# Optimization experiments

Hardware: AMD Instinct MI355X
Metric: run time of the kernel (lower is better)

Reference implementation:

```python
import jax, jax.numpy as jnp
import numpy as np

HIDDEN = 512
NHEADS = 8
ALPHA = 0.1
NUM_HOP = 4
MASK_VAL = -16384.0
LN_EPS = 1e-5


def setup_inputs() -> dict:
    key = jax.random.key(0)
    ks = jax.random.split(key, 10)
    B, N, H = 8, 1024, HIDDEN
    s = 1.0 / np.sqrt(H)
    x = jax.random.normal(ks[0], (B, N, H), dtype=jnp.float32)
    adj = jax.random.randint(ks[1], (B, N, N), 0, 2, dtype=jnp.int32)
    Wq = jax.random.uniform(ks[2], (H, H), jnp.float32, -s, s)
    bq = jax.random.uniform(ks[3], (H,), jnp.float32, -s, s)
    Wk = jax.random.uniform(ks[4], (H, H), jnp.float32, -s, s)
    bk = jax.random.uniform(ks[5], (H,), jnp.float32, -s, s)
    Wv = jax.random.uniform(ks[6], (H, H), jnp.float32, -s, s)
    bv = jax.random.uniform(ks[7], (H,), jnp.float32, -s, s)
    gamma = jnp.ones((H,), jnp.float32)
    beta = jnp.zeros((H,), jnp.float32)
    return {"x": x, "adj": adj, "Wq": Wq, "bq": bq, "Wk": Wk, "bk": bk,
            "Wv": Wv, "bv": bv, "gamma": gamma, "beta": beta}


def reference(x, adj, Wq, bq, Wk, bk, Wv, bv, gamma, beta):
    B, N, H = x.shape
    u = H // NHEADS
    # torch Linear: y = x @ W^T + b
    q = x @ Wq.T + bq  # [B,N,H]
    k = x @ Wk.T + bk
    v = x @ Wv.T + bv
    # split hidden into contiguous head chunks (matches per-head slicing)
    qh = q.reshape(B, N, NHEADS, u).transpose(0, 2, 1, 3)  # [B,Hd,N,u]
    kh = k.reshape(B, N, NHEADS, u).transpose(0, 2, 1, 3)
    vh = v.reshape(B, N, NHEADS, u).transpose(0, 2, 1, 3)
    scores = jnp.einsum('bhnd,bhmd->bhnm', qh, kh)  # [B,Hd,N,N]
    mask = (adj == 0)[:, None, :, :]  # broadcast over heads
    scores = jnp.where(mask, MASK_VAL, scores)
    pros = jax.nn.softmax(scores, axis=-1)
    z_init = vh
    z = z_init
    for _ in range(NUM_HOP):
        z = (1.0 - ALPHA) * jnp.einsum('bhnm,bhmd->bhnd', pros, z) + ALPHA * z_init
    h_prime = z.transpose(0, 2, 1, 3).reshape(B, N, H)  # concat heads
    y = x + h_prime
    mu = jnp.mean(y, axis=-1, keepdims=True)
    var = jnp.mean((y - mu) ** 2, axis=-1, keepdims=True)
    return (y - mu) / jnp.sqrt(var + LN_EPS) * gamma + beta
```

## Files before the change

### kernel.cpp

```cpp
#include <hip/hip_runtime.h>
#include <hip/hip_bf16.h>

#define BB 8
#define NN 1024
#define HH 512
#define NHEADS 8
#define UU 64

typedef __attribute__((ext_vector_type(8))) short short8;
typedef __attribute__((ext_vector_type(4))) float f32x4;
typedef __attribute__((ext_vector_type(16))) float f32x16;
typedef unsigned short u16;
typedef unsigned char u8;

__device__ inline float b2f(unsigned short u) {
    union { float f; unsigned int i; } c; c.i = ((unsigned int)u) << 16; return c.f;
}
__device__ inline unsigned short f2b(float f) {
    __hip_bfloat16 h = __float2bfloat16(f);
    return *reinterpret_cast<unsigned short*>(&h);
}
__device__ inline void gl_lds16(const void* g, void* l) {
    __builtin_amdgcn_global_load_lds(
        (const __attribute__((address_space(1))) unsigned int*)g,
        (__attribute__((address_space(3))) unsigned int*)l, 16, 0, 0);
}

__global__ __launch_bounds__(256) void cvt_w(
    const float* __restrict__ Wq, const float* __restrict__ Wk,
    const float* __restrict__ Wv, u16* __restrict__ Wb)
{
    const int which = blockIdx.y;
    const float* src = which == 0 ? Wq : (which == 1 ? Wk : Wv);
    u16* dst = Wb + (size_t)which * HH * HH;
    const int base = (blockIdx.x * 256 + threadIdx.x) * 8;
    const float4* sp = (const float4*)&src[base];
    float4 a = sp[0], b = sp[1];
    short8 o;
    o[0] = (short)f2b(a.x); o[1] = (short)f2b(a.y);
    o[2] = (short)f2b(a.z); o[3] = (short)f2b(a.w);
    o[4] = (short)f2b(b.x); o[5] = (short)f2b(b.y);
    o[6] = (short)f2b(b.z); o[7] = (short)f2b(b.w);
    *(short8*)&dst[base] = o;
}

__global__ __launch_bounds__(256) void adj_pack(
    const int* __restrict__ adj, unsigned int* __restrict__ adjpT)
{
    const int wave = threadIdx.x >> 6, lane = threadIdx.x & 63;
    const int row = blockIdx.x * 4 + wave;
    const int b = row >> 10, r = row & 1023;
    const int* ar = adj + (size_t)row * NN;
    unsigned int* ob = adjpT + (((size_t)b) << 15) + r;
    #pragma unroll
    for (int it = 0; it < 16; ++it) {
        int a = ar[it * 64 + lane];
        unsigned long long m = __ballot(a != 0);
        if (lane == 0) {
            ob[(size_t)(2 * it)     << 10] = (unsigned int)m;
            ob[(size_t)(2 * it + 1) << 10] = (unsigned int)(m >> 32);
        }
    }
}

__global__ __launch_bounds__(256) void qkv_gemm(
    const float* __restrict__ x, const u16* __restrict__ Wb,
    const float* __restrict__ bq, const float* __restrict__ bk,
    const float* __restrict__ bv,
    u16* __restrict__ q, u16* __restrict__ k, u16* __restrict__ v)
{
    const int which = blockIdx.z;
    const u16* W      = Wb + (size_t)which * HH * HH;
    const float* bias = which == 0 ? bq : (which == 1 ? bk : bv);
    u16* out          = which == 0 ? q  : (which == 1 ? k  : v);

    const int tid = threadIdx.x;
    const int wave = tid >> 6, lane = tid & 63;
    const int ln = lane & 15, quad = lane >> 4;
    const int wr = (wave >> 1) * 64, wc = (wave & 1) * 64;
    const int rowbase = blockIdx.x * 128, colbase = blockIdx.y * 128;

    __shared__ __align__(16) u16 As[128 * 40];
    __shared__ __align__(16) u16 Bs[128 * 32];
    __shared__ __align__(16) u16 Cs[128 * 136];

    f32x4 acc[4][4];
    #pragma unroll
    for (int ri = 0; ri < 4; ++ri)
        #pragma unroll
        for (int ci = 0; ci < 4; ++ci) acc[ri][ci] = (f32x4){0.f, 0.f, 0.f, 0.f};

    const int lr = lane >> 2;
    const int sg = lane & 3;

    for (int kk = 0; kk < HH; kk += 32) {
        __syncthreads();
        #pragma unroll
        for (int i = 0; i < 2; ++i) {
            int r = wave * 32 + i * 16 + lr;
            const float* xp = &x[(size_t)(rowbase + r) * HH + kk + sg * 8];
            float4 f0 = *(const float4*)xp, f1 = *(const float4*)(xp + 4);
            short8 o;
            o[0] = (short)f2b(f0.x); o[1] = (short)f2b(f0.y);
            o[2] = (short)f2b(f0.z); o[3] = (short)f2b(f0.w);
            o[4] = (short)f2b(f1.x); o[5] = (short)f2b(f1.y);
            o[6] = (short)f2b(f1.z); o[7] = (short)f2b(f1.w);
            *(short8*)&As[r * 40 + sg * 8] = o;
            gl_lds16(&W[(size_t)(colbase + r) * HH + kk + sg * 8],
                     (char*)Bs + (wave * 32 + i * 16) * 64);
        }
        __syncthreads();

        short8 bfr[4];
        #pragma unroll
        for (int ci = 0; ci < 4; ++ci)
            bfr[ci] = *(const short8*)&Bs[(wc + ci * 16 + ln) * 32 + quad * 8];
        #pragma unroll
        for (int ri = 0; ri < 4; ++ri) {
            short8 af = *(const short8*)&As[(wr + ri * 16 + ln) * 40 + quad * 8];
            #pragma unroll
            for (int ci = 0; ci < 4; ++ci)
                acc[ri][ci] = __builtin_amdgcn_mfma_f32_16x16x32_bf16(af, bfr[ci], acc[ri][ci], 0, 0, 0);
        }
    }

    #pragma unroll
    for (int ci = 0; ci < 4; ++ci) {
        int col = wc + ci * 16 + ln;
        float bb = bias[colbase + col];
        #pragma unroll
        for (int ri = 0; ri < 4; ++ri) {
            #pragma unroll
            for (int r = 0; r < 4; ++r) {
                int row = wr + ri * 16 + quad * 4 + r;
                Cs[row * 136 + col] = f2b(acc[ri][ci][r] + bb);
            }
        }
    }
    __syncthreads();
    {
        int row = tid >> 1, half = tid & 1;
        int gcol0 = colbase + half * 64;
        int hh = gcol0 >> 6;
        int grow = rowbase + row;
        int bidx = grow >> 10, n = grow & 1023;
        u16* op = &out[(((size_t)(bidx * NHEADS + hh)) * NN + n) * UU];
        const u16* cp = &Cs[row * 136 + half * 64];
        #pragma unroll
        for (int j = 0; j < 8; ++j)
            *(short8*)(op + j * 8) = *(const short8*)(cp + j * 8);
    }
}

__global__ __launch_bounds__(256) void vt8(
    const u16* __restrict__ v, u8* __restrict__ v8t)
{
    const int bh = blockIdx.x >> 2, part = blockIdx.x & 3;
    const int t = threadIdx.x;
    const size_t hd = (size_t)bh << 16;
    __shared__ u16 tile[64][72];

    for (int chunk = part * 4; chunk < part * 4 + 4; ++chunk) {
        const int n0 = chunk * 64;
        const int r = t >> 2, cs = t & 3;
        const u16* vp = &v[((size_t)bh * NN + n0 + r) * UU + cs * 16];
        short8 a = *(const short8*)vp;
        short8 b8 = *(const short8*)(vp + 8);
        #pragma unroll
        for (int j = 0; j < 8; ++j) {
            tile[r][cs * 16 + j] = (u16)a[j];
            tile[r][cs * 16 + 8 + j] = (u16)b8[j];
        }
        __syncthreads();
        const int c = t & 63, qt = t >> 6;
        unsigned int w[4];
        #pragma unroll
        for (int g = 0; g < 4; ++g) {
            float f0 = b2f(tile[qt * 16 + g * 4 + 0][c]);
            float f1 = b2f(tile[qt * 16 + g * 4 + 1][c]);
            float f2 = b2f(tile[qt * 16 + g * 4 + 2][c]);
            float f3 = b2f(tile[qt * 16 + g * 4 + 3][c]);
            int lo = __builtin_amdgcn_cvt_pk_fp8_f32(f0, f1, 0, false);
            w[g] = (unsigned int)__builtin_amdgcn_cvt_pk_fp8_f32(f2, f3, lo, true);
        }
        uint4 o; o.x = w[0]; o.y = w[1]; o.z = w[2]; o.w = w[3];
        *(uint4*)&v8t[hd + (size_t)c * 1024 + n0 + qt * 16] = o;
        __syncthreads();
    }
}

__device__ inline f32x16 score_tile(const u16* kp, unsigned int m2,
                                    const short8* qf)
{
    short8 kf[4];
    #pragma unroll
    for (int f = 0; f < 4; ++f) kf[f] = *(const short8*)(kp + f * 16);
    f32x16 acc;
    #pragma unroll
    for (int j = 0; j < 16; ++j) {
        const int koff = (j & 3) + 8 * (j >> 2);
        acc[j] = ((m2 >> koff) & 1u) ? -32.0f : -16384.0f;
    }
    #pragma unroll
    for (int f = 0; f < 4; ++f)
        acc = __builtin_amdgcn_mfma_f32_32x32x16_bf16(kf[f], qf[f], acc, 0, 0, 0);
    return acc;
}

__global__ __launch_bounds__(256) void scores_softmax(
    const u16* __restrict__ q, const u16* __restrict__ kmat,
    const unsigned int* __restrict__ adjpT, u8* __restrict__ P8)
{
    const int b = blockIdx.z, h = blockIdx.y;
    const int bh = b * NHEADS + h;
    const int tid = threadIdx.x;
    const int wave = tid >> 6, lane = tid & 63;
    const int l31 = lane & 31, hi = lane >> 5;
    const int rg = wave >> 1, kh = wave & 1;
    const int n = (blockIdx.x * 2 + rg) * 32 + l31;
    const int kt0 = kh * 16, kt1 = kt0 + 16;

    __shared__ float rs[2][2][32];

    short8 qf[4];
    const u16* qp = &q[((size_t)bh * NN + n) * UU + hi * 8];
    #pragma unroll
    for (int f = 0; f < 4; ++f) qf[f] = *(const short8*)(qp + f * 16);

    const u16* kbase = kmat + (size_t)bh * NN * UU + hi * 8;
    const unsigned int* mbase = adjpT + (((size_t)b) << 15) + n;

    float rsum = 0.f;
    #pragma unroll 2
    for (int t = kt0; t < kt1; ++t) {
        const unsigned int m2 = mbase[(size_t)t << 10] >> (4 * hi);
        const u16* kp = kbase + (size_t)(t * 32 + l31) * UU;
        f32x16 acc = score_tile(kp, m2, qf);
        #pragma unroll
        for (int j = 0; j < 16; ++j) rsum += __expf(acc[j]);
    }
    rsum += __shfl_xor(rsum, 32);
    if (lane < 32) rs[rg][kh][lane] = rsum;
    __syncthreads();
    const float scl = 16.0f / (rs[rg][0][l31] + rs[rg][1][l31]);

    u8* pb = P8 + (((size_t)bh) << 20) + (size_t)(n >> 4) * 16384
           + (n & 15) * 32 + hi * 4;
    #pragma unroll 2
    for (int t = kt0; t < kt1; ++t) {
        const unsigned int m2 = mbase[(size_t)t << 10] >> (4 * hi);
        const u16* kp = kbase + (size_t)(t * 32 + l31) * UU;
        f32x16 acc = score_tile(kp, m2, qf);
        u8* pt = pb + (size_t)t * 512;
        #pragma unroll
        for (int g = 0; g < 4; ++g) {
            float e0 = __expf(acc[g * 4 + 0]) * scl;
            float e1 = __expf(acc[g * 4 + 1]) * scl;
            float e2 = __expf(acc[g * 4 + 2]) * scl;
            float e3 = __expf(acc[g * 4 + 3]) * scl;
            int lo = __builtin_amdgcn_cvt_pk_fp8_f32(e0, e1, 0, false);
            unsigned int dw = (unsigned int)__builtin_amdgcn_cvt_pk_fp8_f32(e2, e3, lo, true);
            *(unsigned int*)(pt + g * 8) = dw;
        }
    }
}

__global__ __launch_bounds__(512) void hop(
    const u8* __restrict__ P8, const u8* __restrict__ z8in,
    const u16* __restrict__ v, u8* __restrict__ z8out,
    u16* __restrict__ zbf_out, int last)
{
    const int b = blockIdx.z, h = blockIdx.y, rt = blockIdx.x;
    const int bh = b * NHEADS + h;
    const int tid = threadIdx.x;
    const int wave = tid >> 6, lane = tid & 63;
    const int ln = lane & 15, quad = lane >> 4;
    const int wrow = rt * 128 + wave * 16;

    __shared__ __align__(16) u8 zt[64 * 1040];

    const u8* zg = z8in + ((size_t)bh << 16);
    #pragma unroll
    for (int i = 0; i < 8; ++i) {
        int c = wave * 8 + i;
        gl_lds16(zg + (size_t)c * 1024 + lane * 16, (char*)zt + c * 1040);
    }
    __syncthreads();

    f32x4 acc[4];
    #pragma unroll
    for (int ci = 0; ci < 4; ++ci) acc[ci] = (f32x4){0.f, 0.f, 0.f, 0.f};

    const u8* pt = P8 + ((size_t)bh << 20) + (size_t)(rt * 8 + wave) * 16384
                 + ln * 32 + quad * 8;
    #pragma unroll 4
    for (int kc = 0; kc < 32; ++kc) {
        long a = *(const long*)(pt + kc * 512);
        int kk = kc * 32;
        #pragma unroll
        for (int ci = 0; ci < 4; ++ci) {
            long bz = *(const long*)&zt[(ci * 16 + ln) * 1040 + kk + quad * 8];
            acc[ci] = __builtin_amdgcn_mfma_f32_16x16x32_fp8_fp8(a, bz, acc[ci], 0, 0, 0);
        }
    }

    if (last) {
        #pragma unroll
        for (int ci = 0; ci < 4; ++ci) {
            int col = ci * 16 + ln;
            #pragma unroll
            for (int r = 0; r < 4; ++r) {
                int row = wrow + quad * 4 + r;
                float vv = b2f(v[((size_t)bh * NN + row) * UU + col]);
                zbf_out[((size_t)(b * NN + row)) * HH + h * UU + col]
                    = f2b(0.05625f * acc[ci][r] + 0.1f * vv);
            }
        }
    } else {
        u8* zo = z8out + ((size_t)bh << 16);
        #pragma unroll
        for (int ci = 0; ci < 4; ++ci) {
            int col = ci * 16 + ln;
            float zv[4];
            #pragma unroll
            for (int r = 0; r < 4; ++r) {
                int row = wrow + quad * 4 + r;
                float vv = b2f(v[((size_t)bh * NN + row) * UU + col]);
                zv[r] = 0.05625f * acc[ci][r] + 0.1f * vv;
            }
            int lo = __builtin_amdgcn_cvt_pk_fp8_f32(zv[0], zv[1], 0, false);
            unsigned int dw = (unsigned int)__builtin_amdgcn_cvt_pk_fp8_f32(zv[2], zv[3], lo, true);
            *(unsigned int*)&zo[(size_t)col * 1024 + wrow + quad * 4] = dw;
        }
    }
}

__global__ __launch_bounds__(256) void resid_ln(
    const float* __restrict__ x, const u16* __restrict__ z,
    const float* __restrict__ gamma, const float* __restrict__ beta,
    float* __restrict__ out)
{
    const int r = blockIdx.x * 4 + (threadIdx.x >> 6);
    const int lane = threadIdx.x & 63;
    const size_t base = (size_t)r * HH + lane * 8;

    const float4* xp = (const float4*)&x[base];
    float4 x0 = xp[0], x1 = xp[1];
    short8 zv = *(const short8*)&z[base];
    float y[8];
    y[0] = x0.x + b2f((u16)zv[0]); y[1] = x0.y + b2f((u16)zv[1]);
    y[2] = x0.z + b2f((u16)zv[2]); y[3] = x0.w + b2f((u16)zv[3]);
    y[4] = x1.x + b2f((u16)zv[4]); y[5] = x1.y + b2f((u16)zv[5]);
    y[6] = x1.z + b2f((u16)zv[6]); y[7] = x1.w + b2f((u16)zv[7]);

    float s = 0.f, sq = 0.f;
    #pragma unroll
    for (int j = 0; j < 8; ++j) { s += y[j]; sq += y[j] * y[j]; }
    #pragma unroll
    for (int off = 32; off >= 1; off >>= 1) {
        s  += __shfl_xor(s, off);
        sq += __shfl_xor(sq, off);
    }
    const float mu = s * (1.0f / HH);
    const float var = sq * (1.0f / HH) - mu * mu;
    const float rstd = rsqrtf(var + 1e-5f);

    const float4* gp = (const float4*)&gamma[lane * 8];
    const float4* bp = (const float4*)&beta[lane * 8];
    float4 g0 = gp[0], g1 = gp[1], b0 = bp[0], b1 = bp[1];

    float4 o0, o1;
    o0.x = (y[0] - mu) * rstd * g0.x + b0.x;
    o0.y = (y[1] - mu) * rstd * g0.y + b0.y;
    o0.z = (y[2] - mu) * rstd * g0.z + b0.z;
    o0.w = (y[3] - mu) * rstd * g0.w + b0.w;
    o1.x = (y[4] - mu) * rstd * g1.x + b1.x;
    o1.y = (y[5] - mu) * rstd * g1.y + b1.y;
    o1.z = (y[6] - mu) * rstd * g1.z + b1.z;
    o1.w = (y[7] - mu) * rstd * g1.w + b1.w;
    float4* op = (float4*)&out[base];
    op[0] = o0; op[1] = o1;
}

extern "C" void kernel_launch(void* const* d_in, const int* in_sizes, int n_in,
                              void* d_out, int out_size, void* d_ws, size_t ws_size,
                              hipStream_t stream)
{
    const float* x   = (const float*)d_in[0];
    const int* adj   = (const int*)d_in[1];
    const float* Wq  = (const float*)d_in[2];
    const float* bq  = (const float*)d_in[3];
    const float* Wk  = (const float*)d_in[4];
    const float* bk  = (const float*)d_in[5];
    const float* Wv  = (const float*)d_in[6];
    const float* bv  = (const float*)d_in[7];
    const float* gamma = (const float*)d_in[8];
    const float* beta  = (const float*)d_in[9];
    float* out = (float*)d_out;

    const size_t E = (size_t)BB * NN * HH;
    u16* ws16 = (u16*)d_ws;
    u16* q  = ws16 + E;
    u16* k  = ws16 + 2 * E;
    u16* v  = ws16 + 3 * E;
    u16* za = ws16 + 4 * E;
    u16* Wb = ws16 + 5 * E;
    u8* base8 = (u8*)(ws16 + 5 * E + 786432);
    u8* P8  = base8;
    u8* z8a = base8 + ((size_t)64 << 20);
    u8* z8b = z8a + ((size_t)4 << 20);
    u8* v8t = z8b + ((size_t)4 << 20);
    unsigned int* adjpT = (unsigned int*)(v8t + ((size_t)4 << 20));

    cvt_w<<<dim3(128, 3), 256, 0, stream>>>(Wq, Wk, Wv, Wb);
    adj_pack<<<dim3(2048), 256, 0, stream>>>(adj, adjpT);
    qkv_gemm<<<dim3(64, 4, 3), 256, 0, stream>>>(x, Wb, bq, bk, bv, q, k, v);
    vt8<<<dim3(256), 256, 0, stream>>>(v, v8t);
    scores_softmax<<<dim3(16, NHEADS, BB), 256, 0, stream>>>(q, k, adjpT, P8);
    hop<<<dim3(8, NHEADS, BB), 512, 0, stream>>>(P8, v8t, v, z8a, za, 0);
    hop<<<dim3(8, NHEADS, BB), 512, 0, stream>>>(P8, z8a, v, z8b, za, 0);
    hop<<<dim3(8, NHEADS, BB), 512, 0, stream>>>(P8, z8b, v, z8a, za, 0);
    hop<<<dim3(8, NHEADS, BB), 512, 0, stream>>>(P8, z8a, v, z8b, za, 1);
    resid_ln<<<dim3(2048), 256, 0, stream>>>(x, za, gamma, beta, out);
}
```

Baseline: 301.0 us.

## Split softmax rows across four key-quarter waves and use exp2 with folded scaling

The scores_softmax kernel now assigns one 32-row tile per block and splits the keys across four waves instead of two. Each wave preloads its mask words once into registers. The mask and scaling are folded into a single fma+exp2, with the normalisation applied in log space (offset minus log of the row sum), which removes the per-element multiply. Partial sums go into four independent accumulators, and the grid doubles to 32 blocks per head, with a launch bound asking for 8 blocks per CU. This raises parallelism and cuts ALU work, at the cost of more blocks and a log-domain normalisation that slightly changes the rounding.

```diff
diff --git a/kernel.cpp b/kernel.cpp
--- a/kernel.cpp
+++ b/kernel.cpp
@@ -189,77 +189,93 @@
     }
 }
 
-__device__ inline f32x16 score_tile(const u16* kp, unsigned int m2,
-                                    const short8* qf)
+__device__ inline f32x16 score_tile(const u16* kp, const short8* qf)
 {
     short8 kf[4];
     #pragma unroll
     for (int f = 0; f < 4; ++f) kf[f] = *(const short8*)(kp + f * 16);
     f32x16 acc;
     #pragma unroll
-    for (int j = 0; j < 16; ++j) {
-        const int koff = (j & 3) + 8 * (j >> 2);
-        acc[j] = ((m2 >> koff) & 1u) ? -32.0f : -16384.0f;
-    }
+    for (int j = 0; j < 16; ++j) acc[j] = 0.f;
     #pragma unroll
     for (int f = 0; f < 4; ++f)
         acc = __builtin_amdgcn_mfma_f32_32x32x16_bf16(kf[f], qf[f], acc, 0, 0, 0);
     return acc;
 }
 
-__global__ __launch_bounds__(256) void scores_softmax(
+__global__ __launch_bounds__(256, 8) void scores_softmax(
     const u16* __restrict__ q, const u16* __restrict__ kmat,
     const unsigned int* __restrict__ adjpT, u8* __restrict__ P8)
 {
     const int b = blockIdx.z, h = blockIdx.y;
     const int bh = b * NHEADS + h;
     const int tid = threadIdx.x;
-    const int wave = tid >> 6, lane = tid & 63;
+    const int kq = tid >> 6, lane = tid & 63;
     const int l31 = lane & 31, hi = lane >> 5;
-    const int rg = wave >> 1, kh = wave & 1;
-    const int n = (blockIdx.x * 2 + rg) * 32 + l31;
-    const int kt0 = kh * 16, kt1 = kt0 + 16;
-
-    __shared__ float rs[2][2][32];
+    const int n = blockIdx.x * 32 + l31;
+    const int kt0 = kq * 8;
+
+    __shared__ float rs[4][32];
 
     short8 qf[4];
     const u16* qp = &q[((size_t)bh * NN + n) * UU + hi * 8];
     #pragma unroll
     for (int f = 0; f < 4; ++f) qf[f] = *(const short8*)(qp + f * 16);
 
-    const u16* kbase = kmat + (size_t)bh * NN * UU + hi * 8;
+    const u16* kbase = kmat + (size_t)bh * NN * UU + (size_t)(kt0 * 32 + l31) * UU + hi * 8;
     const unsigned int* mbase = adjpT + (((size_t)b) << 15) + n;
 
-    float rsum = 0.f;
+    unsigned int mv[8];
+    #pragma unroll
+    for (int i = 0; i < 8; ++i)
+        mv[i] = mbase[(size_t)(kt0 + i) << 10] >> (4 * hi);
+
+    const float L2E = 1.442695041f;
+    const float C0 = -46.16624f;
+    const float CM = -100000.0f;
+
+    float rs0 = 0.f, rs1 = 0.f, rs2 = 0.f, rs3 = 0.f;
     #pragma unroll 2
-    for (int t = kt0; t < kt1; ++t) {
-        const unsigned int m2 = mbase[(size_t)t << 10] >> (4 * hi);
-        const u16* kp = kbase + (size_t)(t * 32 + l31) * UU;
-        f32x16 acc = score_tile(kp, m2, qf);
-        #pragma unroll
-        for (int j = 0; j < 16; ++j) rsum += __expf(acc[j]);
-    }
+    for (int i = 0; i < 8; ++i) {
+        f32x16 acc = score_tile(kbase + (size_t)i * (32 * UU), qf);
+        const unsigned int m2 = mv[i];
+        #pragma unroll
+        for (int g = 0; g < 4; ++g) {
+            #pragma unroll
+            for (int r = 0; r < 4; ++r) {
+                const int koff = r + 8 * g;
+                float addv = ((m2 >> koff) & 1u) ? C0 : CM;
+                float e = __builtin_amdgcn_exp2f(fmaf(L2E, acc[g * 4 + r], addv));
+                if (g == 0) rs0 += e; else if (g == 1) rs1 += e;
+                else if (g == 2) rs2 += e; else rs3 += e;
+            }
+        }
+    }
+    float rsum = (rs0 + rs1) + (rs2 + rs3);
     rsum += __shfl_xor(rsum, 32);
-    if (lane < 32) rs[rg][kh][lane] = rsum;
+    if (lane < 32) rs[kq][lane] = rsum;
     __syncthreads();
-    const float scl = 16.0f / (rs[rg][0][l31] + rs[rg][1][l31]);
+    const float total = (rs[0][l31] + rs[1][l31]) + (rs[2][l31] + rs[3][l31]);
+    const float lscl = -42.16624f - __builtin_amdgcn_logf(total);
 
     u8* pb = P8 + (((size_t)bh) << 20) + (size_t)(n >> 4) * 16384
            + (n & 15) * 32 + hi * 4;
     #pragma unroll 2
-    for (int t = kt0; t < kt1; ++t) {
-        const unsigned int m2 = mbase[(size_t)t << 10] >> (4 * hi);
-        const u16* kp = kbase + (size_t)(t * 32 + l31) * UU;
-        f32x16 acc = score_tile(kp, m2, qf);
-        u8* pt = pb + (size_t)t * 512;
+    for (int i = 0; i < 8; ++i) {
+        f32x16 acc = score_tile(kbase + (size_t)i * (32 * UU), qf);
+        const unsigned int m2 = mv[i];
+        u8* pt = pb + (size_t)(kt0 + i) * 512;
         #pragma unroll
         for (int g = 0; g < 4; ++g) {
-            float e0 = __expf(acc[g * 4 + 0]) * scl;
-            float e1 = __expf(acc[g * 4 + 1]) * scl;
-            float e2 = __expf(acc[g * 4 + 2]) * scl;
-            float e3 = __expf(acc[g * 4 + 3]) * scl;
-            int lo = __builtin_amdgcn_cvt_pk_fp8_f32(e0, e1, 0, false);
-            unsigned int dw = (unsigned int)__builtin_amdgcn_cvt_pk_fp8_f32(e2, e3, lo, true);
+            float e[4];
+            #pragma unroll
+            for (int r = 0; r < 4; ++r) {
+                const int koff = r + 8 * g;
+                float addv = ((m2 >> koff) & 1u) ? lscl : CM;
+                e[r] = __builtin_amdgcn_exp2f(fmaf(L2E, acc[g * 4 + r], addv));
+            }
+            int lo = __builtin_amdgcn_cvt_pk_fp8_f32(e[0], e[1], 0, false);
+            unsigned int dw = (unsigned int)__builtin_amdgcn_cvt_pk_fp8_f32(e[2], e[3], lo, true);
             *(unsigned int*)(pt + g * 8) = dw;
         }
     }
@@ -416,7 +432,7 @@
     adj_pack<<<dim3(2048), 256, 0, stream>>>(adj, adjpT);
     qkv_gemm<<<dim3(64, 4, 3), 256, 0, stream>>>(x, Wb, bq, bk, bv, q, k, v);
     vt8<<<dim3(256), 256, 0, stream>>>(v, v8t);
-    scores_softmax<<<dim3(16, NHEADS, BB), 256, 0, stream>>>(q, k, adjpT, P8);
+    scores_softmax<<<dim3(32, NHEADS, BB), 256, 0, stream>>>(q, k, adjpT, P8);
     hop<<<dim3(8, NHEADS, BB), 512, 0, stream>>>(P8, v8t, v, z8a, za, 0);
     hop<<<dim3(8, NHEADS, BB), 512, 0, stream>>>(P8, z8a, v, z8b, za, 0);
     hop<<<dim3(8, NHEADS, BB), 512, 0, stream>>>(P8, z8b, v, z8a, za, 0);
```

Measured after the change: 445.9 us. +48.1%, slower.
